# Kernel optimization log

Hardware: AMD Instinct MI355X
Metric: run time of the kernel (lower is better)

The kernel has to match this reference:

```python
import jax, jax.numpy as jnp
import numpy as np

D_MODEL = 1024
NUM_HEADS = 16
D_K = D_MODEL // NUM_HEADS
FFN_SIZE = 4096
EPS = 1e-6


def _layer_norm(x, gamma, beta):
    mu = jnp.mean(x, axis=-1, keepdims=True)
    var = jnp.var(x, axis=-1, keepdims=True)
    return (x - mu) / jnp.sqrt(var + EPS) * gamma + beta


def setup_inputs() -> dict:
    key = jax.random.key(0)
    ks = jax.random.split(key, 12)
    B, S = 2, 2048
    s_attn = 1.0 / np.sqrt(D_MODEL)
    s_ffn1 = 1.0 / np.sqrt(D_MODEL)
    s_ffn2 = 1.0 / np.sqrt(FFN_SIZE)
    return {
        "x": jax.random.normal(ks[0], (B, S, D_MODEL), dtype=jnp.float32),
        "W_q": jax.random.normal(ks[1], (D_MODEL, D_MODEL), dtype=jnp.float32) * s_attn,
        "W_k": jax.random.normal(ks[2], (D_MODEL, D_MODEL), dtype=jnp.float32) * s_attn,
        "W_v": jax.random.normal(ks[3], (D_MODEL, D_MODEL), dtype=jnp.float32) * s_attn,
        "W_o": jax.random.normal(ks[4], (D_MODEL, D_MODEL), dtype=jnp.float32) * s_attn,
        "b_o": jnp.zeros((D_MODEL,), dtype=jnp.float32),
        "W1": jax.random.normal(ks[5], (D_MODEL, FFN_SIZE), dtype=jnp.float32) * s_ffn1,
        "b1": jnp.zeros((FFN_SIZE,), dtype=jnp.float32),
        "W2": jax.random.normal(ks[6], (FFN_SIZE, D_MODEL), dtype=jnp.float32) * s_ffn2,
        "b2": jnp.zeros((D_MODEL,), dtype=jnp.float32),
        "ln1_g": jnp.ones((D_MODEL,), dtype=jnp.float32),
        "ln1_b": jnp.zeros((D_MODEL,), dtype=jnp.float32),
        "ln2_g": jnp.ones((D_MODEL,), dtype=jnp.float32),
        "ln2_b": jnp.zeros((D_MODEL,), dtype=jnp.float32),
    }


def reference(x, W_q, W_k, W_v, W_o, b_o, W1, b1, W2, b2,
              ln1_g, ln1_b, ln2_g, ln2_b):
    B, S, _ = x.shape

    # --- self-attention sublayer (pre-norm residual) ---
    h = _layer_norm(x, ln1_g, ln1_b)
    q = (h @ W_q).reshape(B, S, NUM_HEADS, D_K).transpose(0, 2, 1, 3)  # [B,H,S,Dk]
    k = (h @ W_k).reshape(B, S, NUM_HEADS, D_K).transpose(0, 2, 1, 3)
    v = (h @ W_v).reshape(B, S, NUM_HEADS, D_K).transpose(0, 2, 1, 3)
    scores = jnp.einsum("bhqd,bhkd->bhqk", q, k) / jnp.sqrt(jnp.float32(D_K))
    attn = jax.nn.softmax(scores, axis=-1)
    ctx = jnp.einsum("bhqk,bhkd->bhqd", attn, v)
    ctx = ctx.transpose(0, 2, 1, 3).reshape(B, S, D_MODEL)
    x = x + (ctx @ W_o + b_o)

    # --- FFN sublayer (pre-norm residual) ---
    h2 = _layer_norm(x, ln2_g, ln2_b)
    f = jax.nn.relu(h2 @ W1 + b1) @ W2 + b2
    return x + f
```

## Files before the change

### kernel.cpp

```cpp
#include <hip/hip_runtime.h>
#include <cstdint>
#include <cstddef>


typedef __attribute__((ext_vector_type(8))) __bf16 bf16x8;
typedef __attribute__((ext_vector_type(4))) __bf16 bf16x4;
typedef __attribute__((ext_vector_type(4))) float f32x4;

__device__ __forceinline__ void async16(const void* g, void* l) {
  __builtin_amdgcn_global_load_lds(
      (__attribute__((address_space(1))) void*)g,
      (__attribute__((address_space(3))) void*)l, 16, 0, 0);
}

__device__ __forceinline__ f32x4 mfma16(bf16x8 a, bf16x8 b, f32x4 c) {
  return __builtin_amdgcn_mfma_f32_16x16x32_bf16(a, b, c, 0, 0, 0);
}

template <int N>
__device__ __forceinline__ void wait_vmcnt() {
  if constexpr (N == 0) {
    asm volatile("s_waitcnt vmcnt(0)" ::: "memory");
  } else if constexpr (N == 3) {
    asm volatile("s_waitcnt vmcnt(3)" ::: "memory");
  } else {
    asm volatile("s_waitcnt vmcnt(4)" ::: "memory");
  }
}
__device__ __forceinline__ void barrier_raw() {
  asm volatile("s_barrier" ::: "memory");
}

__global__ __launch_bounds__(256) void transpose_all(
    const float* __restrict__ Wq, const float* __restrict__ Wk,
    const float* __restrict__ Wv, const float* __restrict__ Wo,
    const float* __restrict__ W1, const float* __restrict__ W2,
    __bf16* __restrict__ WqkvT, __bf16* __restrict__ WoT,
    __bf16* __restrict__ W1T, __bf16* __restrict__ W2T) {
  const int id = blockIdx.x;
  const float* in;
  __bf16* out;
  int ld_in, ld_out, c0, r0;
  if (id < 1024) {
    const int which = id >> 8, tl = id & 255;
    c0 = (tl & 15) * 64;
    r0 = (tl >> 4) * 64;
    ld_in = 1024;
    ld_out = 1024;
    if (which == 0) { in = Wq; out = WqkvT; }
    else if (which == 1) { in = Wk; out = WqkvT + 1048576; }
    else if (which == 2) { in = Wv; out = WqkvT + 2097152; }
    else { in = Wo; out = WoT; }
  } else if (id < 2048) {
    const int tl = id - 1024;
    c0 = (tl & 63) * 64;
    r0 = (tl >> 6) * 64;
    in = W1; out = W1T; ld_in = 4096; ld_out = 1024;
  } else {
    const int tl = id - 2048;
    c0 = (tl & 15) * 64;
    r0 = (tl >> 4) * 64;
    in = W2; out = W2T; ld_in = 1024; ld_out = 4096;
  }
  __shared__ __bf16 tile[64][65];
  const int tx = threadIdx.x & 63, ty = threadIdx.x >> 6;
#pragma unroll
  for (int i = 0; i < 16; i++) {
    int r = ty + i * 4;
    tile[r][tx] = (__bf16)in[(size_t)(r0 + r) * ld_in + c0 + tx];
  }
  __syncthreads();
#pragma unroll
  for (int i = 0; i < 16; i++) {
    int r = ty + i * 4;
    out[(size_t)(c0 + r) * ld_out + r0 + tx] = tile[tx][r];
  }
}

__global__ __launch_bounds__(256) void transpose_bf16(
    const unsigned short* __restrict__ in, unsigned short* __restrict__ out,
    int ld_in, int ld_out) {
  __shared__ unsigned short tile[64][65];
  const int c0 = blockIdx.x * 64, r0 = blockIdx.y * 64;
  const int tx = threadIdx.x & 63, ty = threadIdx.x >> 6;
#pragma unroll
  for (int i = 0; i < 16; i++) {
    int r = ty + i * 4;
    tile[r][tx] = in[(size_t)(r0 + r) * ld_in + c0 + tx];
  }
  __syncthreads();
#pragma unroll
  for (int i = 0; i < 16; i++) {
    int r = ty + i * 4;
    out[(size_t)(c0 + r) * ld_out + r0 + tx] = tile[tx][r];
  }
}

__global__ __launch_bounds__(256) void ln_kernel(
    const float* __restrict__ xin, const float* __restrict__ g,
    const float* __restrict__ bt, __bf16* __restrict__ out) {
  const int tok = blockIdx.x * 4 + (threadIdx.x >> 6);
  const int lane = threadIdx.x & 63;
  const int base0 = lane * 8, base1 = 512 + lane * 8;
  const float* xr = xin + (size_t)tok * 1024;
  float v[16];
  float4 a0 = *(const float4*)(xr + base0);
  float4 a1 = *(const float4*)(xr + base0 + 4);
  float4 a2 = *(const float4*)(xr + base1);
  float4 a3 = *(const float4*)(xr + base1 + 4);
  v[0] = a0.x; v[1] = a0.y; v[2] = a0.z; v[3] = a0.w;
  v[4] = a1.x; v[5] = a1.y; v[6] = a1.z; v[7] = a1.w;
  v[8] = a2.x; v[9] = a2.y; v[10] = a2.z; v[11] = a2.w;
  v[12] = a3.x; v[13] = a3.y; v[14] = a3.z; v[15] = a3.w;
  float s = 0.f, s2 = 0.f;
#pragma unroll
  for (int i = 0; i < 16; i++) { s += v[i]; s2 += v[i] * v[i]; }
#pragma unroll
  for (int m = 1; m < 64; m <<= 1) {
    s += __shfl_xor(s, m);
    s2 += __shfl_xor(s2, m);
  }
  const float mean = s * (1.f / 1024.f);
  const float var = s2 * (1.f / 1024.f) - mean * mean;
  const float rstd = rsqrtf(var + 1e-6f);
  float4 g0 = *(const float4*)(g + base0), g1 = *(const float4*)(g + base0 + 4);
  float4 g2 = *(const float4*)(g + base1), g3 = *(const float4*)(g + base1 + 4);
  float4 b0 = *(const float4*)(bt + base0), b1v = *(const float4*)(bt + base0 + 4);
  float4 b2v = *(const float4*)(bt + base1), b3 = *(const float4*)(bt + base1 + 4);
  float gg[16] = {g0.x, g0.y, g0.z, g0.w, g1.x, g1.y, g1.z, g1.w,
                  g2.x, g2.y, g2.z, g2.w, g3.x, g3.y, g3.z, g3.w};
  float bb[16] = {b0.x, b0.y, b0.z, b0.w, b1v.x, b1v.y, b1v.z, b1v.w,
                  b2v.x, b2v.y, b2v.z, b2v.w, b3.x, b3.y, b3.z, b3.w};
  bf16x8 o0, o1;
#pragma unroll
  for (int j = 0; j < 8; j++) {
    o0[j] = (__bf16)((v[j] - mean) * rstd * gg[j] + bb[j]);
    o1[j] = (__bf16)((v[8 + j] - mean) * rstd * gg[8 + j] + bb[8 + j]);
  }
  __bf16* op = out + (size_t)tok * 1024;
  *(bf16x8*)(op + base0) = o0;
  *(bf16x8*)(op + base1) = o1;
}

template <int EPI, int TM, int SPLITS = 1>
__global__ __launch_bounds__(256) void gemm_bt(
    const __bf16* __restrict__ A, int lda, const __bf16* __restrict__ BT,
    int ldb, void* __restrict__ C, int ldc, int Kb,
    const float* __restrict__ bias, const float* __restrict__ res, int ldres) {
  const int t = threadIdx.x;
  const int m0 = blockIdx.x * TM, n0 = blockIdx.y * 128;
  const int kz = (SPLITS > 1) ? blockIdx.z : 0;
  __shared__ __align__(16) __bf16 As[3][TM * 32];
  __shared__ __align__(16) __bf16 Bs[3][128 * 32];
  const int lane = t & 63, w = t >> 6;
  const int quad = lane >> 4, l15 = lane & 15;
  const int wm = w >> 1, wn = w & 1;
  constexpr int MF = TM / 32;
  constexpr int LOADS = TM / 64 + 2;

  f32x4 acc[MF][4] = {};

  const int swc = ((t & 3) ^ ((t >> 3) & 3)) * 8;
  const __bf16* ga = A + (size_t)(m0 + (t >> 2)) * lda + swc + (size_t)kz * Kb;
  const __bf16* gb = BT + (size_t)(n0 + (t >> 2)) * ldb + swc + (size_t)kz * Kb;
  const size_t a64 = (size_t)64 * lda, b64 = (size_t)64 * ldb;

  auto stage = [&](int buf) {
#pragma unroll
    for (int i = 0; i < TM / 64; i++)
      async16(ga + i * a64, As[buf] + t * 8 + i * 2048);
    async16(gb, Bs[buf] + t * 8);
    async16(gb + b64, Bs[buf] + t * 8 + 2048);
    ga += 32;
    gb += 32;
  };
  const int ce = (quad ^ ((l15 >> 1) & 3)) * 8;
  auto compute = [&](int buf) {
    bf16x8 af[MF], bfr[4];
#pragma unroll
    for (int i = 0; i < MF; i++)
      af[i] = *(const bf16x8*)&As[buf][(wm * (TM / 2) + i * 16 + l15) * 32 + ce];
#pragma unroll
    for (int i = 0; i < 4; i++)
      bfr[i] = *(const bf16x8*)&Bs[buf][(wn * 64 + i * 16 + l15) * 32 + ce];
#pragma unroll
    for (int mi = 0; mi < MF; mi++)
#pragma unroll
      for (int ni = 0; ni < 4; ni++)
        acc[mi][ni] = mfma16(af[mi], bfr[ni], acc[mi][ni]);
  };

  const int iters = Kb / 32;
  stage(0);
  stage(1);
  int cur = 0, stg = 2;
  for (int it = 0; it < iters - 1; ++it) {
    wait_vmcnt<LOADS>();
    barrier_raw();
    if (it + 2 < iters) stage(stg);
    compute(cur);
    cur = (cur == 2) ? 0 : cur + 1;
    stg = (stg == 2) ? 0 : stg + 1;
  }
  wait_vmcnt<0>();
  barrier_raw();
  compute(cur);

  float biasv[4];
  if constexpr (EPI != 0) {
#pragma unroll
    for (int ni = 0; ni < 4; ni++)
      biasv[ni] = bias[n0 + wn * 64 + ni * 16 + l15];
  }
  __bf16* Cb = (__bf16*)C;
  if constexpr (SPLITS > 1)
    Cb += (size_t)kz * gridDim.x * TM * ldc;
#pragma unroll
  for (int mi = 0; mi < MF; mi++)
#pragma unroll
    for (int ni = 0; ni < 4; ni++)
#pragma unroll
      for (int r = 0; r < 4; r++) {
        const int row = m0 + wm * (TM / 2) + mi * 16 + quad * 4 + r;
        const int col = n0 + wn * 64 + ni * 16 + l15;
        float v = acc[mi][ni][r];
        if constexpr (EPI == 0) {
          Cb[(size_t)row * ldc + col] = (__bf16)v;
        } else if constexpr (EPI == 1) {
          v += biasv[ni] + res[(size_t)row * ldres + col];
          ((float*)C)[(size_t)row * ldc + col] = v;
        } else {
          v += biasv[ni];
          ((__bf16*)C)[(size_t)row * ldc + col] = (__bf16)fmaxf(v, 0.f);
        }
      }
}

__global__ __launch_bounds__(256) void reduce_split(
    const __bf16* __restrict__ P, const float* __restrict__ bias,
    const float* __restrict__ res, float* __restrict__ out) {
  const int row = blockIdx.x, c = threadIdx.x * 4;
  const size_t i = (size_t)row * 1024 + c;
  bf16x4 p0 = *(const bf16x4*)(P + i);
  bf16x4 p1 = *(const bf16x4*)(P + 4194304 + i);
  float4 r = *(const float4*)(res + i);
  float4 bv = *(const float4*)(bias + c);
  float4 o;
  o.x = (float)p0[0] + (float)p1[0] + r.x + bv.x;
  o.y = (float)p0[1] + (float)p1[1] + r.y + bv.y;
  o.z = (float)p0[2] + (float)p1[2] + r.z + bv.z;
  o.w = (float)p0[3] + (float)p1[3] + r.w + bv.w;
  *(float4*)(out + i) = o;
}

__global__ __launch_bounds__(256, 2) void attn_kernel(
    const __bf16* __restrict__ QKV, const __bf16* __restrict__ VT,
    __bf16* __restrict__ ctx) {
  const int qt = blockIdx.x, bh = blockIdx.y;
  const int b = bh >> 4, h = bh & 15;
  const int t = threadIdx.x, w = t >> 6, lane = t & 63;
  const int quad = lane >> 4, l15 = lane & 15;
  const int tok0 = b * 2048;
  const int q0w = tok0 + qt * 128 + w * 32;

  __shared__ __align__(16) __bf16 Ks[2][128 * 64];
  __shared__ __align__(16) __bf16 VTs[2][64 * 128];

  const float qs = 0.18033688011112042f;
  bf16x8 qf[2][2];
#pragma unroll
  for (int mi = 0; mi < 2; mi++)
#pragma unroll
    for (int kb = 0; kb < 2; kb++) {
      const __bf16* src = QKV + (size_t)(q0w + mi * 16 + l15) * 3072 + h * 64 +
                          kb * 32 + quad * 8;
      bf16x8 r = *(const bf16x8*)src;
#pragma unroll
      for (int j = 0; j < 8; j++) r[j] = (__bf16)((float)r[j] * qs);
      qf[mi][kb] = r;
    }

  f32x4 lacc[2] = {};
  f32x4 O[2][4] = {};

  const int krow = t >> 3;
  const int kcg = (((t & 7) ^ (krow & 7)) * 8);
  const int vrow = t >> 4;
  const int vcg = (((2 * (t & 15)) ^ ((vrow & 7) * 2)) * 4);
  const int sub = 4 * (quad & 1);
  const int qh = quad >> 1;

  auto stage = [&](int buf, int kt) {
    const int ktok = tok0 + kt * 128;
#pragma unroll
    for (int j = 0; j < 4; j++) {
      const __bf16* gp =
          QKV + (size_t)(ktok + krow + j * 32) * 3072 + 1024 + h * 64 + kcg;
      async16(gp, Ks[buf] + t * 8 + j * 2048);
    }
#pragma unroll
    for (int j = 0; j < 4; j++) {
      const __bf16* gp =
          VT + (size_t)(h * 64 + vrow + j * 16) * 4096 + ktok + vcg;
      async16(gp, VTs[buf] + t * 8 + j * 2048);
    }
  };

  stage(0, 0);
  wait_vmcnt<0>();
  barrier_raw();

  int buf = 0;
  for (int kt = 0; kt < 16; ++kt) {
    if (kt + 1 < 16) stage(buf ^ 1, kt + 1);

    f32x4 sT[2][8];
#pragma unroll
    for (int kt8 = 0; kt8 < 8; kt8++) {
      f32x4 a0 = {}, a1 = {};
#pragma unroll
      for (int kb = 0; kb < 2; kb++) {
        bf16x8 kf = *(const bf16x8*)&Ks[buf][(kt8 * 16 + l15) * 64 +
                                            (((kb * 4 + quad) ^ (l15 & 7)) * 8)];
        a0 = mfma16(kf, qf[0][kb], a0);
        a1 = mfma16(kf, qf[1][kb], a1);
      }
      sT[0][kt8] = a0;
      sT[1][kt8] = a1;
    }

    bf16x8 pf[2][4];
#pragma unroll
    for (int mi = 0; mi < 2; mi++)
#pragma unroll
      for (int kb = 0; kb < 4; kb++)
#pragma unroll
        for (int hf = 0; hf < 2; hf++)
#pragma unroll
          for (int r = 0; r < 4; r++) {
            const float p = __builtin_amdgcn_exp2f(sT[mi][2 * kb + hf][r]);
            lacc[mi][r] += p;
            pf[mi][kb][hf * 4 + r] = (__bf16)p;
          }

#pragma unroll
    for (int kb = 0; kb < 4; kb++) {
      const int g0 = (((4 * kb + qh) ^ (l15 & 7)) * 8) + sub;
      const int g1 = (((4 * kb + 2 + qh) ^ (l15 & 7)) * 8) + sub;
#pragma unroll
      for (int nd = 0; nd < 4; nd++) {
        const int base = (nd * 16 + l15) * 128;
        bf16x4 a0 = *(const bf16x4*)&VTs[buf][base + g0];
        bf16x4 a1 = *(const bf16x4*)&VTs[buf][base + g1];
        bf16x8 vf;
        vf[0] = a0[0]; vf[1] = a0[1]; vf[2] = a0[2]; vf[3] = a0[3];
        vf[4] = a1[0]; vf[5] = a1[1]; vf[6] = a1[2]; vf[7] = a1[3];
        O[0][nd] = mfma16(pf[0][kb], vf, O[0][nd]);
        O[1][nd] = mfma16(pf[1][kb], vf, O[1][nd]);
      }
    }

    wait_vmcnt<0>();
    barrier_raw();
    buf ^= 1;
  }

#pragma unroll
  for (int mi = 0; mi < 2; mi++) {
    float lsum = lacc[mi][0] + lacc[mi][1] + lacc[mi][2] + lacc[mi][3];
    lsum += __shfl_xor(lsum, 16);
    lsum += __shfl_xor(lsum, 32);
    float rl[4];
#pragma unroll
    for (int r = 0; r < 4; r++) rl[r] = 1.0f / __shfl(lsum, quad * 4 + r);
#pragma unroll
    for (int nd = 0; nd < 4; nd++)
#pragma unroll
      for (int r = 0; r < 4; r++) {
        const int tokq = q0w + mi * 16 + quad * 4 + r;
        const int col = h * 64 + nd * 16 + l15;
        ctx[(size_t)tokq * 1024 + col] = (__bf16)(O[mi][nd][r] * rl[r]);
      }
  }
}

extern "C" void kernel_launch(void* const* d_in, const int* in_sizes, int n_in,
                              void* d_out, int out_size, void* d_ws,
                              size_t ws_size, hipStream_t stream) {
  (void)in_sizes; (void)n_in; (void)out_size; (void)ws_size;

  const float* x = (const float*)d_in[0];
  const float* Wq = (const float*)d_in[1];
  const float* Wk = (const float*)d_in[2];
  const float* Wv = (const float*)d_in[3];
  const float* Wo = (const float*)d_in[4];
  const float* b_o = (const float*)d_in[5];
  const float* W1 = (const float*)d_in[6];
  const float* b1 = (const float*)d_in[7];
  const float* W2 = (const float*)d_in[8];
  const float* b2 = (const float*)d_in[9];
  const float* ln1g = (const float*)d_in[10];
  const float* ln1b = (const float*)d_in[11];
  const float* ln2g = (const float*)d_in[12];
  const float* ln2b = (const float*)d_in[13];

  char* ws = (char*)d_ws;
  __bf16* WqkvT = (__bf16*)(ws + 0);
  __bf16* WoT = (__bf16*)(ws + 6291456);
  __bf16* W1T = (__bf16*)(ws + 8388608);
  __bf16* W2T = (__bf16*)(ws + 16777216);
  __bf16* h = (__bf16*)(ws + 25165824);
  __bf16* QKV = (__bf16*)(ws + 33554432);
  __bf16* VT = (__bf16*)(ws + 58720256);
  __bf16* ctx = (__bf16*)(ws + 67108864);
  float* x1 = (float*)(ws + 75497472);
  __bf16* f1 = QKV;
  __bf16* Pw2 = (__bf16*)(ws + 0);

  const dim3 blk(256);

  transpose_all<<<dim3(3072), blk, 0, stream>>>(Wq, Wk, Wv, Wo, W1, W2, WqkvT,
                                                WoT, W1T, W2T);

  ln_kernel<<<dim3(1024), blk, 0, stream>>>(x, ln1g, ln1b, h);

  gemm_bt<0, 128><<<dim3(32, 24), blk, 0, stream>>>(
      h, 1024, WqkvT, 1024, (void*)QKV, 3072, 1024, nullptr, nullptr, 0);

  transpose_bf16<<<dim3(16, 64), blk, 0, stream>>>(
      (const unsigned short*)(QKV + 2048), (unsigned short*)VT, 3072, 4096);

  attn_kernel<<<dim3(16, 32), blk, 0, stream>>>(QKV, VT, ctx);

  gemm_bt<1, 64><<<dim3(64, 8), blk, 0, stream>>>(
      ctx, 1024, WoT, 1024, (void*)x1, 1024, 1024, b_o, x, 1024);

  ln_kernel<<<dim3(1024), blk, 0, stream>>>(x1, ln2g, ln2b, h);

  gemm_bt<2, 128><<<dim3(32, 32), blk, 0, stream>>>(
      h, 1024, W1T, 1024, (void*)f1, 4096, 1024, b1, nullptr, 0);

  gemm_bt<0, 128, 2><<<dim3(32, 8, 2), blk, 0, stream>>>(
      f1, 4096, W2T, 4096, (void*)Pw2, 1024, 2048, nullptr, nullptr, 0);
  reduce_split<<<dim3(4096), blk, 0, stream>>>(Pw2, b2, x1, (float*)d_out);
}
```

Measured before the change: 341.8 us.

## Add 256x256-tile 512-thread GEMM with interleaved LDS staging for QKV and FFN

Adds a new GEMM kernel using 256x256 output tiles, 8 waves, swizzled LDS, and a quarter-tile interleaved async load/compute schedule with raised wave priority around MFMAs. It replaces the 128-tile GEMMs for the QKV projection, FFN1, and FFN2. FFN2 moves from a 2-way to a 4-way K split, with a matching 4-way reduction. The workspace layout is rearranged to fit the larger partial buffer. The aim is more operand reuse per LDS load and less global traffic, at the cost of fewer blocks per grid (192/256 blocks on 256 CUs) and more bf16 partial-sum rounding.

```diff
diff --git a/kernel.cpp b/kernel.cpp
--- a/kernel.cpp
+++ b/kernel.cpp
@@ -29,6 +29,9 @@
 }
 __device__ __forceinline__ void barrier_raw() {
   asm volatile("s_barrier" ::: "memory");
+}
+__device__ __forceinline__ void lgkm0() {
+  asm volatile("s_waitcnt lgkmcnt(0)" ::: "memory");
 }
 
 __global__ __launch_bounds__(256) void transpose_all(
@@ -142,6 +145,147 @@
   *(bf16x8*)(op + base1) = o1;
 }
 
+template <int EPI, int SPLITS = 1>
+__global__ __launch_bounds__(512, 2) void gemm256(
+    const __bf16* __restrict__ A, int lda, const __bf16* __restrict__ BT,
+    int ldb, void* __restrict__ C, int ldc, int Kb,
+    const float* __restrict__ bias) {
+  const int t = threadIdx.x;
+  const int m0 = blockIdx.x * 256, n0 = blockIdx.y * 256;
+  const int kz = (SPLITS > 1) ? blockIdx.z : 0;
+  __shared__ __align__(16) __bf16 As[2][2][8192];
+  __shared__ __align__(16) __bf16 Bs[2][2][8192];
+  const int lane = t & 63;
+  const int quad = lane >> 4, l15 = lane & 15;
+  const int w = t >> 6, wm = w >> 2, wn = w & 3;
+
+  f32x4 acc[8][4] = {};
+
+  const int rr = t >> 3;
+  const int ca = (t & 7) ^ (rr & 7);
+  const int cc = rr & 31;
+  const int wnb = t >> 8;
+  const int cb = (t & 7) ^ (cc & 7);
+  const __bf16* gA = A + (size_t)kz * Kb + (size_t)(m0 + rr) * lda + ca * 8;
+  const __bf16* gB = BT + (size_t)kz * Kb +
+                     (size_t)(n0 + wnb * 64 + cc) * ldb + cb * 8;
+  const size_t a64 = (size_t)64 * lda, a128 = (size_t)128 * lda;
+  const size_t b32 = (size_t)32 * ldb, b128 = (size_t)128 * ldb;
+
+  auto stageA = [&](int buf, int mq, int ko) {
+    const __bf16* g = gA + (mq ? a64 : 0) + ko;
+    __bf16* l = &As[buf][mq][t * 8];
+    async16(g, l);
+    async16(g + a128, l + 4096);
+  };
+  auto stageB = [&](int buf, int nq, int ko) {
+    const __bf16* g = gB + (nq ? b32 : 0) + ko;
+    __bf16* l = &Bs[buf][nq][t * 8];
+    async16(g, l);
+    async16(g + b128, l + 4096);
+  };
+
+  const int arow = wm * 4096 + l15 * 64;
+  const int brow = wn * 2048 + l15 * 64;
+  const int x7 = l15 & 7;
+
+  auto loadA = [&](int buf, int mq, bf16x8 (&af)[4][2]) {
+#pragma unroll
+    for (int mi = 0; mi < 4; mi++)
+#pragma unroll
+      for (int kk = 0; kk < 2; kk++)
+        af[mi][kk] = *(const bf16x8*)&As[buf][mq]
+            [arow + mi * 1024 + (((kk * 4 + quad) ^ x7) * 8)];
+  };
+  auto loadB = [&](int buf, int nq, bf16x8 (&bv)[2][2]) {
+#pragma unroll
+    for (int ni = 0; ni < 2; ni++)
+#pragma unroll
+      for (int kk = 0; kk < 2; kk++)
+        bv[ni][kk] = *(const bf16x8*)&Bs[buf][nq]
+            [brow + ni * 1024 + (((kk * 4 + quad) ^ x7) * 8)];
+  };
+  auto mm = [&](int mq, int nq, const bf16x8 (&af)[4][2],
+                const bf16x8 (&bv)[2][2]) {
+    __builtin_amdgcn_s_setprio(1);
+#pragma unroll
+    for (int mi = 0; mi < 4; mi++)
+#pragma unroll
+      for (int ni = 0; ni < 2; ni++)
+#pragma unroll
+        for (int kk = 0; kk < 2; kk++)
+          acc[mq * 4 + mi][nq * 2 + ni] =
+              mfma16(af[mi][kk], bv[ni][kk], acc[mq * 4 + mi][nq * 2 + ni]);
+    __builtin_amdgcn_s_setprio(0);
+  };
+
+  const int NT = Kb / 64;
+  stageA(0, 0, 0); stageB(0, 0, 0); stageA(0, 1, 0); stageB(0, 1, 0);
+  stageA(1, 0, 64); stageB(1, 0, 64);
+  wait_vmcnt<4>();
+  barrier_raw();
+
+  bf16x8 af[4][2], b0[2][2], b1[2][2];
+  for (int s = 0; s < NT; ++s) {
+    const int buf = s & 1;
+    const int ko1 = (s + 1) * 64, ko2 = (s + 2) * 64;
+    loadA(buf, 0, af);
+    loadB(buf, 0, b0);
+    if (s + 1 < NT) stageA(buf ^ 1, 1, ko1);
+    barrier_raw();
+    lgkm0();
+    mm(0, 0, af, b0);
+    barrier_raw();
+    loadB(buf, 1, b1);
+    if (s + 1 < NT) stageB(buf ^ 1, 1, ko1);
+    barrier_raw();
+    lgkm0();
+    mm(0, 1, af, b1);
+    barrier_raw();
+    loadA(buf, 1, af);
+    if (s + 2 < NT) stageA(buf, 0, ko2);
+    barrier_raw();
+    lgkm0();
+    mm(1, 0, af, b0);
+    barrier_raw();
+    if (s + 2 < NT) {
+      stageB(buf, 0, ko2);
+      wait_vmcnt<4>();
+    } else {
+      wait_vmcnt<0>();
+    }
+    barrier_raw();
+    mm(1, 1, af, b1);
+    barrier_raw();
+  }
+
+  float biasv[4];
+  if constexpr (EPI == 2) {
+#pragma unroll
+    for (int ni = 0; ni < 4; ni++)
+      biasv[ni] = bias[n0 + wn * 64 + ni * 16 + l15];
+  }
+  __bf16* Cb = (__bf16*)C;
+  if constexpr (SPLITS > 1)
+    Cb += (size_t)kz * (size_t)gridDim.x * 256 * ldc;
+#pragma unroll
+  for (int mi = 0; mi < 8; mi++)
+#pragma unroll
+    for (int ni = 0; ni < 4; ni++)
+#pragma unroll
+      for (int r = 0; r < 4; r++) {
+        const int row = m0 + wm * 128 + mi * 16 + quad * 4 + r;
+        const int col = n0 + wn * 64 + ni * 16 + l15;
+        float v = acc[mi][ni][r];
+        if constexpr (EPI == 0) {
+          Cb[(size_t)row * ldc + col] = (__bf16)v;
+        } else {
+          v += biasv[ni];
+          Cb[(size_t)row * ldc + col] = (__bf16)fmaxf(v, 0.f);
+        }
+      }
+}
+
 template <int EPI, int TM, int SPLITS = 1>
 __global__ __launch_bounds__(256) void gemm_bt(
     const __bf16* __restrict__ A, int lda, const __bf16* __restrict__ BT,
@@ -236,20 +380,23 @@
       }
 }
 
-__global__ __launch_bounds__(256) void reduce_split(
+__global__ __launch_bounds__(256) void reduce_split4(
     const __bf16* __restrict__ P, const float* __restrict__ bias,
     const float* __restrict__ res, float* __restrict__ out) {
   const int row = blockIdx.x, c = threadIdx.x * 4;
   const size_t i = (size_t)row * 1024 + c;
-  bf16x4 p0 = *(const bf16x4*)(P + i);
-  bf16x4 p1 = *(const bf16x4*)(P + 4194304 + i);
   float4 r = *(const float4*)(res + i);
   float4 bv = *(const float4*)(bias + c);
-  float4 o;
-  o.x = (float)p0[0] + (float)p1[0] + r.x + bv.x;
-  o.y = (float)p0[1] + (float)p1[1] + r.y + bv.y;
-  o.z = (float)p0[2] + (float)p1[2] + r.z + bv.z;
-  o.w = (float)p0[3] + (float)p1[3] + r.w + bv.w;
+  float s0 = r.x + bv.x, s1 = r.y + bv.y, s2 = r.z + bv.z, s3 = r.w + bv.w;
+#pragma unroll
+  for (int j = 0; j < 4; j++) {
+    bf16x4 p = *(const bf16x4*)(P + (size_t)j * 4194304 + i);
+    s0 += (float)p[0];
+    s1 += (float)p[1];
+    s2 += (float)p[2];
+    s3 += (float)p[3];
+  }
+  float4 o = {s0, s1, s2, s3};
   *(float4*)(out + i) = o;
 }
 
@@ -405,27 +552,28 @@
   const float* ln2b = (const float*)d_in[13];
 
   char* ws = (char*)d_ws;
-  __bf16* WqkvT = (__bf16*)(ws + 0);
-  __bf16* WoT = (__bf16*)(ws + 6291456);
+  __bf16* h = (__bf16*)(ws + 0);
   __bf16* W1T = (__bf16*)(ws + 8388608);
-  __bf16* W2T = (__bf16*)(ws + 16777216);
-  __bf16* h = (__bf16*)(ws + 25165824);
-  __bf16* QKV = (__bf16*)(ws + 33554432);
-  __bf16* VT = (__bf16*)(ws + 58720256);
-  __bf16* ctx = (__bf16*)(ws + 67108864);
-  float* x1 = (float*)(ws + 75497472);
-  __bf16* f1 = QKV;
+  __bf16* WqkvT = (__bf16*)(ws + 16777216);
+  __bf16* WoT = (__bf16*)(ws + 23068672);
+  __bf16* QKV = (__bf16*)(ws + 25165824);
+  __bf16* VT = (__bf16*)(ws + 50331648);
+  __bf16* ctx = (__bf16*)(ws + 58720256);
+  __bf16* f1 = (__bf16*)(ws + 33554432);
   __bf16* Pw2 = (__bf16*)(ws + 0);
+  float* x1 = (float*)(ws + 67108864);
+  __bf16* W2T = (__bf16*)(ws + 83886080);
 
   const dim3 blk(256);
+  const dim3 blk512(512);
 
   transpose_all<<<dim3(3072), blk, 0, stream>>>(Wq, Wk, Wv, Wo, W1, W2, WqkvT,
                                                 WoT, W1T, W2T);
 
   ln_kernel<<<dim3(1024), blk, 0, stream>>>(x, ln1g, ln1b, h);
 
-  gemm_bt<0, 128><<<dim3(32, 24), blk, 0, stream>>>(
-      h, 1024, WqkvT, 1024, (void*)QKV, 3072, 1024, nullptr, nullptr, 0);
+  gemm256<0><<<dim3(16, 12), blk512, 0, stream>>>(
+      h, 1024, WqkvT, 1024, (void*)QKV, 3072, 1024, nullptr);
 
   transpose_bf16<<<dim3(16, 64), blk, 0, stream>>>(
       (const unsigned short*)(QKV + 2048), (unsigned short*)VT, 3072, 4096);
@@ -437,10 +585,10 @@
 
   ln_kernel<<<dim3(1024), blk, 0, stream>>>(x1, ln2g, ln2b, h);
 
-  gemm_bt<2, 128><<<dim3(32, 32), blk, 0, stream>>>(
-      h, 1024, W1T, 1024, (void*)f1, 4096, 1024, b1, nullptr, 0);
-
-  gemm_bt<0, 128, 2><<<dim3(32, 8, 2), blk, 0, stream>>>(
-      f1, 4096, W2T, 4096, (void*)Pw2, 1024, 2048, nullptr, nullptr, 0);
-  reduce_split<<<dim3(4096), blk, 0, stream>>>(Pw2, b2, x1, (float*)d_out);
-}
+  gemm256<2><<<dim3(16, 16), blk512, 0, stream>>>(
+      h, 1024, W1T, 1024, (void*)f1, 4096, 1024, b1);
+
+  gemm256<0, 4><<<dim3(16, 4, 4), blk512, 0, stream>>>(
+      f1, 4096, W2T, 4096, (void*)Pw2, 1024, 1024, nullptr);
+  reduce_split4<<<dim3(4096), blk, 0, stream>>>(Pw2, b2, x1, (float*)d_out);
+}
```

After: 320.5 us. 1.07x faster.
